# Kernel optimization log

Hardware: AMD Instinct MI355X
Metric: run time of the kernel (lower is better)

The kernel has to match this reference:

```python
import jax, jax.numpy as jnp
import numpy as np


def setup_inputs() -> dict:
    key = jax.random.key(0)
    ks = jax.random.split(key, 5)
    B, N, L, d = 8, 2048, 2048, 512
    q = N // 4
    return {
        "logits": jax.random.normal(ks[0], (B, N, L), jnp.float32),
        "emb0": jax.random.normal(ks[1], (q, d), jnp.float32),
        "emb1": jax.random.normal(ks[2], (q, d), jnp.float32),
        "emb2": jax.random.normal(ks[3], (q, d), jnp.float32),
        "emb3": jax.random.normal(ks[4], (q, d), jnp.float32),
    }


def reference(logits, emb0, emb1, emb2, emb3):
    # Eval / late-epoch path of Embedding.forward (process_block_max, k=3):
    # per head: top-k over codebook dim -> masked softmax -> einsum combine.
    # softmax over only the top-k values is mathematically identical to
    # softmax of the -inf-masked full logits, and gathering the k codebook
    # rows is identical to the dense einsum 'bnl,nm->bml' with that sparse attn.
    K = 3
    B, N, L = logits.shape
    E = jnp.stack([emb0, emb1, emb2, emb3])            # (4, q, d)
    q = E.shape[1]
    lg = logits.reshape(B, 4, q, L).transpose(0, 1, 3, 2)  # (B, 4, L, q)
    vals, idx = jax.lax.top_k(lg, K)                   # (B, 4, L, K)
    w = jax.nn.softmax(vals, axis=-1)                  # sparse attn weights

    def head(emb_h, idx_h, w_h):
        g = emb_h[idx_h]                               # (B, L, K, d) gather
        return jnp.einsum('blk,blkd->bld', w_h, g)     # (B, L, d)

    outs = jax.vmap(head, in_axes=(0, 1, 1))(E, idx, w)  # (4, B, L, d)
    # output = out_0 + out_1 + out_2 + out_3, returned as (B, d, L)
    return outs.sum(axis=0).transpose(0, 2, 1)
```

## Files before the change

kernel.cpp:

```cpp
#include <hip/hip_runtime.h>
#include <math.h>

#define BB 8
#define NN 2048
#define LL 2048
#define QQ 512
#define DD 512

__device__ __forceinline__ void top3_insert(float v, int i, float& m0,
                                            float& m1, float& m2, int& j0,
                                            int& j1, int& j2) {
  bool gt0 = v > m0, gt1 = v > m1, gt2 = v > m2;
  float nv2 = gt1 ? m1 : (gt2 ? v : m2);
  int   ni2 = gt1 ? j1 : (gt2 ? i : j2);
  float nv1 = gt0 ? m0 : (gt1 ? v : m1);
  int   ni1 = gt0 ? j0 : (gt1 ? i : j1);
  m0 = gt0 ? v : m0;
  j0 = gt0 ? i : j0;
  m1 = nv1; j1 = ni1; m2 = nv2; j2 = ni2;
}

__global__ __launch_bounds__(256) void topk_part_kernel(
    const float* __restrict__ logits, float4* __restrict__ part) {
  const int u     = threadIdx.x & 63;
  const int g     = threadIdx.x >> 6;
  const int lt    = blockIdx.x;
  const int h     = blockIdx.y;
  const int b     = blockIdx.z >> 2;
  const int ns    = blockIdx.z & 3;
  const int chunk = ns * 4 + g;
  const int n0    = chunk * 32;
  const int l4    = lt * 256 + u * 4;

  const float* base = logits + ((size_t)(b * NN + h * QQ + n0) * LL) + l4;

  float v0[4], v1[4], v2[4];
  int   i0[4], i1[4], i2[4];
#pragma unroll
  for (int j = 0; j < 4; ++j) {
    v0[j] = v1[j] = v2[j] = -INFINITY;
    i0[j] = i1[j] = i2[j] = 0;
  }

  float4 buf[8];
  for (int t = 0; t < 4; ++t) {
#pragma unroll
    for (int p = 0; p < 8; ++p)
      buf[p] = *(const float4*)(base + (size_t)(t * 8 + p) * LL);
#pragma unroll
    for (int p = 0; p < 8; ++p) {
      const int i = n0 + t * 8 + p;
      top3_insert(buf[p].x, i, v0[0], v1[0], v2[0], i0[0], i1[0], i2[0]);
      top3_insert(buf[p].y, i, v0[1], v1[1], v2[1], i0[1], i1[1], i2[1]);
      top3_insert(buf[p].z, i, v0[2], v1[2], v2[2], i0[2], i1[2], i2[2]);
      top3_insert(buf[p].w, i, v0[3], v1[3], v2[3], i0[3], i1[3], i2[3]);
    }
  }

  float4* pout = part + ((size_t)((b * 4 + h) * 16 + chunk)) * LL + l4;
#pragma unroll
  for (int j = 0; j < 4; ++j) {
    unsigned int pi = (unsigned int)i0[j] | ((unsigned int)i1[j] << 9) |
                      ((unsigned int)i2[j] << 18);
    pout[j] = make_float4(v0[j], v1[j], v2[j], __uint_as_float(pi));
  }
}

__global__ __launch_bounds__(256) void combine_kernel(
    const float4* __restrict__ part,
    const float* __restrict__ emb0, const float* __restrict__ emb1,
    const float* __restrict__ emb2, const float* __restrict__ emb3,
    float* __restrict__ out) {
  const int u    = threadIdx.x & 63;
  const int w    = threadIdx.x >> 6;
  const int lblk = blockIdx.x * 16;
  const int b    = blockIdx.y;

  __shared__ float wt_s[4][16][3];
  __shared__ int   rid_s[4][16][3];
  __shared__ float tile[16][516];

  if (threadIdx.x < 64) {
    const int h  = threadIdx.x >> 4;
    const int il = threadIdx.x & 15;
    const int l  = lblk + il;
    const float4* pp = part + ((size_t)(b * 4 + h) * 16) * LL + l;

    float m0 = -INFINITY, m1 = -INFINITY, m2 = -INFINITY;
    int   j0 = 0, j1 = 0, j2 = 0;
#pragma unroll
    for (int c = 0; c < 16; ++c) {
      float4 P = pp[(size_t)c * LL];
      unsigned int pi = __float_as_uint(P.w);
      top3_insert(P.x, pi & 511, m0, m1, m2, j0, j1, j2);
      top3_insert(P.y, (pi >> 9) & 511, m0, m1, m2, j0, j1, j2);
      top3_insert(P.z, (pi >> 18) & 511, m0, m1, m2, j0, j1, j2);
    }
    float e1 = __expf(m1 - m0), e2 = __expf(m2 - m0);
    float inv = 1.0f / (1.0f + e1 + e2);
    wt_s[h][il][0] = inv;
    wt_s[h][il][1] = e1 * inv;
    wt_s[h][il][2] = e2 * inv;
    rid_s[h][il][0] = j0;
    rid_s[h][il][1] = j1;
    rid_s[h][il][2] = j2;
  }
  __syncthreads();

  const float* embs[4] = {emb0, emb1, emb2, emb3};

#pragma unroll
  for (int il = 0; il < 4; ++il) {
    const int ll = w * 4 + il;
    float wt[12];
    const float* rows[12];
#pragma unroll
    for (int h = 0; h < 4; ++h) {
#pragma unroll
      for (int k = 0; k < 3; ++k) {
        wt[h * 3 + k]   = wt_s[h][ll][k];
        rows[h * 3 + k] = embs[h] + (size_t)rid_s[h][ll][k] * DD;
      }
    }
#pragma unroll
    for (int p = 0; p < 2; ++p) {
      const int d = p * 256 + u * 4;
      float a0 = 0.f, a1 = 0.f, a2 = 0.f, a3 = 0.f;
#pragma unroll
      for (int m = 0; m < 12; ++m) {
        const float4 e = *(const float4*)(rows[m] + d);
        a0 += wt[m] * e.x;
        a1 += wt[m] * e.y;
        a2 += wt[m] * e.z;
        a3 += wt[m] * e.w;
      }
      *(float4*)&tile[ll][d] = make_float4(a0, a1, a2, a3);
    }
  }
  __syncthreads();

  const int l0  = (threadIdx.x & 3) * 4;
  const int dof = threadIdx.x >> 2;
  float* outb = out + (size_t)b * DD * LL + lblk + l0;
#pragma unroll
  for (int dd = 0; dd < 512; dd += 64) {
    const int d = dd + dof;
    float4 r;
    r.x = tile[l0 + 0][d];
    r.y = tile[l0 + 1][d];
    r.z = tile[l0 + 2][d];
    r.w = tile[l0 + 3][d];
    *(float4*)(outb + (size_t)d * LL) = r;
  }
}

extern "C" void kernel_launch(void* const* d_in, const int* in_sizes, int n_in,
                              void* d_out, int out_size, void* d_ws,
                              size_t ws_size, hipStream_t stream) {
  const float* logits = (const float*)d_in[0];
  const float* emb0   = (const float*)d_in[1];
  const float* emb1   = (const float*)d_in[2];
  const float* emb2   = (const float*)d_in[3];
  const float* emb3   = (const float*)d_in[4];
  float*       out    = (float*)d_out;
  float4*      part   = (float4*)d_ws;

  dim3 ga(8, 4, 32);
  topk_part_kernel<<<ga, 256, 0, stream>>>(logits, part);

  dim3 gb(LL / 16, BB);
  combine_kernel<<<gb, 256, 0, stream>>>(part, emb0, emb1, emb2, emb3, out);
}
```

Baseline: 232.1 us.

## Fuse top-k partial scan and embedding combine into a single kernel

Replaces the two-kernel pipeline (partial top-3 written to global workspace, then a merge and combine kernel) with one fused kernel per 32-column L tile. Partial top-3 results are now reduced through shared memory with tie-aware merging, and the combine and transposed store are done in two D halves to cut tile shared memory. This removes the workspace round trip and one launch. In exchange, the logits reads become narrower float2 loads with fewer blocks (512 blocks of 512 threads), which may lower memory-level parallelism.

```diff
diff --git a/kernel.cpp b/kernel.cpp
--- a/kernel.cpp
+++ b/kernel.cpp
@@ -2,7 +2,6 @@
 #include <math.h>
 
 #define BB 8
-#define NN 2048
 #define LL 2048
 #define QQ 512
 #define DD 512
@@ -20,137 +19,150 @@
   m1 = nv1; j1 = ni1; m2 = nv2; j2 = ni2;
 }
 
-__global__ __launch_bounds__(256) void topk_part_kernel(
-    const float* __restrict__ logits, float4* __restrict__ part) {
-  const int u     = threadIdx.x & 63;
-  const int g     = threadIdx.x >> 6;
-  const int lt    = blockIdx.x;
-  const int h     = blockIdx.y;
-  const int b     = blockIdx.z >> 2;
-  const int ns    = blockIdx.z & 3;
-  const int chunk = ns * 4 + g;
-  const int n0    = chunk * 32;
-  const int l4    = lt * 256 + u * 4;
-
-  const float* base = logits + ((size_t)(b * NN + h * QQ + n0) * LL) + l4;
-
-  float v0[4], v1[4], v2[4];
-  int   i0[4], i1[4], i2[4];
-#pragma unroll
-  for (int j = 0; j < 4; ++j) {
-    v0[j] = v1[j] = v2[j] = -INFINITY;
-    i0[j] = i1[j] = i2[j] = 0;
-  }
-
-  float4 buf[8];
-  for (int t = 0; t < 4; ++t) {
-#pragma unroll
-    for (int p = 0; p < 8; ++p)
-      buf[p] = *(const float4*)(base + (size_t)(t * 8 + p) * LL);
-#pragma unroll
-    for (int p = 0; p < 8; ++p) {
-      const int i = n0 + t * 8 + p;
-      top3_insert(buf[p].x, i, v0[0], v1[0], v2[0], i0[0], i1[0], i2[0]);
-      top3_insert(buf[p].y, i, v0[1], v1[1], v2[1], i0[1], i1[1], i2[1]);
-      top3_insert(buf[p].z, i, v0[2], v1[2], v2[2], i0[2], i1[2], i2[2]);
-      top3_insert(buf[p].w, i, v0[3], v1[3], v2[3], i0[3], i1[3], i2[3]);
-    }
-  }
-
-  float4* pout = part + ((size_t)((b * 4 + h) * 16 + chunk)) * LL + l4;
-#pragma unroll
-  for (int j = 0; j < 4; ++j) {
-    unsigned int pi = (unsigned int)i0[j] | ((unsigned int)i1[j] << 9) |
-                      ((unsigned int)i2[j] << 18);
-    pout[j] = make_float4(v0[j], v1[j], v2[j], __uint_as_float(pi));
-  }
+__device__ __forceinline__ void top3_tie(float v, int i, float& m0, float& m1,
+                                         float& m2, int& j0, int& j1,
+                                         int& j2) {
+  bool b0 = (v > m0) || ((v == m0) && (i < j0));
+  bool b1 = (v > m1) || ((v == m1) && (i < j1));
+  bool b2 = (v > m2) || ((v == m2) && (i < j2));
+  float nv2 = b1 ? m1 : (b2 ? v : m2);
+  int   nj2 = b1 ? j1 : (b2 ? i : j2);
+  float nv1 = b0 ? m0 : (b1 ? v : m1);
+  int   nj1 = b0 ? j0 : (b1 ? i : j1);
+  m0 = b0 ? v : m0;
+  j0 = b0 ? i : j0;
+  m1 = nv1; j1 = nj1; m2 = nv2; j2 = nj2;
 }
 
-__global__ __launch_bounds__(256) void combine_kernel(
-    const float4* __restrict__ part,
+__global__ __launch_bounds__(512, 4) void fused_kernel(
+    const float* __restrict__ logits,
     const float* __restrict__ emb0, const float* __restrict__ emb1,
     const float* __restrict__ emb2, const float* __restrict__ emb3,
     float* __restrict__ out) {
-  const int u    = threadIdx.x & 63;
-  const int w    = threadIdx.x >> 6;
-  const int lblk = blockIdx.x * 16;
-  const int b    = blockIdx.y;
+  const int t  = threadIdx.x;
+  const int u  = t & 63;
+  const int g  = t >> 6;
+  const int lt = blockIdx.x;
+  const int b  = blockIdx.y;
+  const int l0 = lt * 32;
 
-  __shared__ float wt_s[4][16][3];
-  __shared__ int   rid_s[4][16][3];
-  __shared__ float tile[16][516];
+  __shared__ float          sv[4 * 8 * 32 * 3];
+  __shared__ unsigned short si[4 * 8 * 32 * 3];
+  __shared__ float          tile[32 * 260];
+  __shared__ float          wt_s[4][32][3];
+  __shared__ int            rid_s[4][32][3];
 
-  if (threadIdx.x < 64) {
-    const int h  = threadIdx.x >> 4;
-    const int il = threadIdx.x & 15;
-    const int l  = lblk + il;
-    const float4* pp = part + ((size_t)(b * 4 + h) * 16) * LL + l;
+  {
+    const int h  = g >> 1;
+    const int s  = g & 1;
+    const int p  = u >> 4;
+    const int lp = u & 15;
+    const float2* base = (const float2*)(
+        logits + ((size_t)((b * 4 + h) * QQ + s * 256 + p) * LL) + l0 + lp * 2);
 
+    float v0[2], v1[2], v2[2];
+    int   i0[2], i1[2], i2[2];
+#pragma unroll
+    for (int j = 0; j < 2; ++j) {
+      v0[j] = v1[j] = v2[j] = -INFINITY;
+      i0[j] = i1[j] = i2[j] = 0;
+    }
+
+    float2 buf[8];
+    for (int batch = 0; batch < 8; ++batch) {
+#pragma unroll
+      for (int j = 0; j < 8; ++j)
+        buf[j] = base[(size_t)(batch * 8 + j) * (LL * 2)];
+#pragma unroll
+      for (int j = 0; j < 8; ++j) {
+        const int q = s * 256 + (batch * 8 + j) * 4 + p;
+        top3_insert(buf[j].x, q, v0[0], v1[0], v2[0], i0[0], i1[0], i2[0]);
+        top3_insert(buf[j].y, q, v0[1], v1[1], v2[1], i0[1], i1[1], i2[1]);
+      }
+    }
+
+    const int sp = s * 4 + p;
+#pragma unroll
+    for (int j = 0; j < 2; ++j) {
+      const int li = lp * 2 + j;
+      const int bi = ((h * 8 + sp) * 32 + li) * 3;
+      sv[bi + 0] = v0[j]; sv[bi + 1] = v1[j]; sv[bi + 2] = v2[j];
+      si[bi + 0] = (unsigned short)i0[j];
+      si[bi + 1] = (unsigned short)i1[j];
+      si[bi + 2] = (unsigned short)i2[j];
+    }
+  }
+  __syncthreads();
+
+  if (t < 128) {
+    const int h  = t >> 5;
+    const int li = t & 31;
     float m0 = -INFINITY, m1 = -INFINITY, m2 = -INFINITY;
     int   j0 = 0, j1 = 0, j2 = 0;
 #pragma unroll
-    for (int c = 0; c < 16; ++c) {
-      float4 P = pp[(size_t)c * LL];
-      unsigned int pi = __float_as_uint(P.w);
-      top3_insert(P.x, pi & 511, m0, m1, m2, j0, j1, j2);
-      top3_insert(P.y, (pi >> 9) & 511, m0, m1, m2, j0, j1, j2);
-      top3_insert(P.z, (pi >> 18) & 511, m0, m1, m2, j0, j1, j2);
+    for (int sp = 0; sp < 8; ++sp) {
+      const int bi = ((h * 8 + sp) * 32 + li) * 3;
+#pragma unroll
+      for (int k = 0; k < 3; ++k)
+        top3_tie(sv[bi + k], (int)si[bi + k], m0, m1, m2, j0, j1, j2);
     }
     float e1 = __expf(m1 - m0), e2 = __expf(m2 - m0);
     float inv = 1.0f / (1.0f + e1 + e2);
-    wt_s[h][il][0] = inv;
-    wt_s[h][il][1] = e1 * inv;
-    wt_s[h][il][2] = e2 * inv;
-    rid_s[h][il][0] = j0;
-    rid_s[h][il][1] = j1;
-    rid_s[h][il][2] = j2;
+    wt_s[h][li][0] = inv;
+    wt_s[h][li][1] = e1 * inv;
+    wt_s[h][li][2] = e2 * inv;
+    rid_s[h][li][0] = j0 * DD;
+    rid_s[h][li][1] = j1 * DD;
+    rid_s[h][li][2] = j2 * DD;
   }
   __syncthreads();
 
   const float* embs[4] = {emb0, emb1, emb2, emb3};
+  for (int dh = 0; dh < 2; ++dh) {
+#pragma unroll
+    for (int j = 0; j < 4; ++j) {
+      const int li = g * 4 + j;
+      float wt[12];
+      int   off[12];
+#pragma unroll
+      for (int h = 0; h < 4; ++h)
+#pragma unroll
+        for (int k = 0; k < 3; ++k) {
+          wt[h * 3 + k]  = wt_s[h][li][k];
+          off[h * 3 + k] = rid_s[h][li][k];
+        }
+      const int d = dh * 256 + u * 4;
+      float a0 = 0.f, a1 = 0.f, a2 = 0.f, a3 = 0.f;
+#pragma unroll
+      for (int h = 0; h < 4; ++h) {
+        const float* eb = embs[h];
+#pragma unroll
+        for (int k = 0; k < 3; ++k) {
+          const float4 e = *(const float4*)(eb + off[h * 3 + k] + d);
+          const float wv = wt[h * 3 + k];
+          a0 += wv * e.x; a1 += wv * e.y; a2 += wv * e.z; a3 += wv * e.w;
+        }
+      }
+      *(float4*)&tile[li * 260 + u * 4] = make_float4(a0, a1, a2, a3);
+    }
+    __syncthreads();
 
+    {
+      const int lg  = t & 7;
+      const int dof = t >> 3;
+      float* outb = out + (size_t)b * DD * LL + l0 + lg * 4;
 #pragma unroll
-  for (int il = 0; il < 4; ++il) {
-    const int ll = w * 4 + il;
-    float wt[12];
-    const float* rows[12];
-#pragma unroll
-    for (int h = 0; h < 4; ++h) {
-#pragma unroll
-      for (int k = 0; k < 3; ++k) {
-        wt[h * 3 + k]   = wt_s[h][ll][k];
-        rows[h * 3 + k] = embs[h] + (size_t)rid_s[h][ll][k] * DD;
+      for (int dd = 0; dd < 4; ++dd) {
+        const int dl = dd * 64 + dof;
+        float4 r;
+        r.x = tile[(lg * 4 + 0) * 260 + dl];
+        r.y = tile[(lg * 4 + 1) * 260 + dl];
+        r.z = tile[(lg * 4 + 2) * 260 + dl];
+        r.w = tile[(lg * 4 + 3) * 260 + dl];
+        *(float4*)(outb + (size_t)(dh * 256 + dl) * LL) = r;
       }
     }
-#pragma unroll
-    for (int p = 0; p < 2; ++p) {
-      const int d = p * 256 + u * 4;
-      float a0 = 0.f, a1 = 0.f, a2 = 0.f, a3 = 0.f;
-#pragma unroll
-      for (int m = 0; m < 12; ++m) {
-        const float4 e = *(const float4*)(rows[m] + d);
-        a0 += wt[m] * e.x;
-        a1 += wt[m] * e.y;
-        a2 += wt[m] * e.z;
-        a3 += wt[m] * e.w;
-      }
-      *(float4*)&tile[ll][d] = make_float4(a0, a1, a2, a3);
-    }
-  }
-  __syncthreads();
-
-  const int l0  = (threadIdx.x & 3) * 4;
-  const int dof = threadIdx.x >> 2;
-  float* outb = out + (size_t)b * DD * LL + lblk + l0;
-#pragma unroll
-  for (int dd = 0; dd < 512; dd += 64) {
-    const int d = dd + dof;
-    float4 r;
-    r.x = tile[l0 + 0][d];
-    r.y = tile[l0 + 1][d];
-    r.z = tile[l0 + 2][d];
-    r.w = tile[l0 + 3][d];
-    *(float4*)(outb + (size_t)d * LL) = r;
+    __syncthreads();
   }
 }
 
@@ -163,11 +175,7 @@
   const float* emb2   = (const float*)d_in[3];
   const float* emb3   = (const float*)d_in[4];
   float*       out    = (float*)d_out;
-  float4*      part   = (float4*)d_ws;
 
-  dim3 ga(8, 4, 32);
-  topk_part_kernel<<<ga, 256, 0, stream>>>(logits, part);
-
-  dim3 gb(LL / 16, BB);
-  combine_kernel<<<gb, 256, 0, stream>>>(part, emb0, emb1, emb2, emb3, out);
+  dim3 grid(LL / 32, BB);
+  fused_kernel<<<grid, 512, 0, stream>>>(logits, emb0, emb1, emb2, emb3, out);
 }
```

After: 236.3 us. About the same (+1.8%).
